# Kernel optimization log

Hardware: AMD Instinct MI355X
Metric: run time of the kernel (lower is better)

The kernel has to match this reference:

```python
import jax, jax.numpy as jnp
import numpy as np

N_NODES = 100000


def gcn_conv(x, src, dst, norm, W, b, n_nodes):
    # x: [N, Din]; src/dst: [E'] (with self-loops); norm: [E']
    h = x @ W  # [N, Dout] dense transform first (PyG GCNConv order)
    msgs = h[src] * norm[:, None]  # gather + degree scaling, [E', Dout]
    out = jax.ops.segment_sum(msgs, dst, num_segments=n_nodes)  # scatter-add
    return out + b


def setup_inputs() -> dict:
    key = jax.random.key(0)
    k_x, k_e, k_w1, k_w2 = jax.random.split(key, 4)
    input_dim, hidden_dim = 256, 128
    n_edges = 1600000
    x = jax.random.normal(k_x, (N_NODES, input_dim), dtype=jnp.float32)
    edge_index = jax.random.randint(k_e, (2, n_edges), 0, N_NODES, dtype=jnp.int64)
    # Glorot-style init for conv weights, zeros bias (PyG defaults)
    s1 = (6.0 / (input_dim + hidden_dim)) ** 0.5
    s2 = (6.0 / (hidden_dim + hidden_dim)) ** 0.5
    W1 = jax.random.uniform(k_w1, (input_dim, hidden_dim), jnp.float32, -s1, s1)
    W2 = jax.random.uniform(k_w2, (hidden_dim, hidden_dim), jnp.float32, -s2, s2)
    b1 = jnp.zeros((hidden_dim,), jnp.float32)
    b2 = jnp.zeros((hidden_dim,), jnp.float32)
    return {"x": x, "edge_index": edge_index, "W1": W1, "b1": b1, "W2": W2, "b2": b2}


def reference(x, edge_index, W1, b1, W2, b2):
    n = x.shape[0]
    loops = jnp.arange(n, dtype=edge_index.dtype)
    src = jnp.concatenate([edge_index[0], loops])  # add self-loops
    dst = jnp.concatenate([edge_index[1], loops])
    # symmetric normalization deg^-1/2 (in-degree including self-loops)
    deg = jax.ops.segment_sum(jnp.ones_like(dst, dtype=x.dtype), dst, num_segments=n)
    dinv = jax.lax.rsqrt(deg)
    norm = dinv[src] * dinv[dst]
    # layer 1: GCNConv -> ReLU (dropout is identity in eval mode)
    h = jax.nn.relu(gcn_conv(x, src, dst, norm, W1, b1, n))
    # layer 2
    h = jax.nn.relu(gcn_conv(h, src, dst, norm, W2, b2, n))
    return h
```

## Files before the change

kernel.cpp:

```cpp
#include <hip/hip_runtime.h>
#include <hip/hip_bf16.h>


#define DIN 256
#define DH 128
#define BKT_SHIFT 9
#define BKT_SZ 512
#define NBKT_MAX 256
#define CAP 10240

typedef __attribute__((ext_vector_type(8))) short short8;
typedef __attribute__((ext_vector_type(4))) float f32x4;
typedef __attribute__((ext_vector_type(2))) unsigned int uint2e;

__device__ __forceinline__ unsigned short f2bf(float f) {
    union { float f; unsigned int i; } c;
    c.f = f;
    unsigned int r = c.i + 0x7FFFu + ((c.i >> 16) & 1u);
    return (unsigned short)(r >> 16);
}
__device__ __forceinline__ float bf_lo(unsigned int u) {
    union { unsigned int i; float f; } c;
    c.i = u << 16;
    return c.f;
}
__device__ __forceinline__ float bf_hi(unsigned int u) {
    union { unsigned int i; float f; } c;
    c.i = u & 0xFFFF0000u;
    return c.f;
}

__global__ __launch_bounds__(256) void cvt_zero_k(const float* __restrict__ W1,
                                                  const float* __restrict__ W2,
                                                  unsigned short* __restrict__ Wt1,
                                                  unsigned short* __restrict__ Wt2,
                                                  int* __restrict__ bcnt, int WTB) {
    int bx = blockIdx.x;
    int t = threadIdx.x;
    if (bx >= WTB) {
        bcnt[t] = 0;
        return;
    }
    int i = bx * 256 + t;
    if (i < 256 * 128) {
        int k = i >> 7, nn = i & 127;
        Wt1[(size_t)nn * 256 + k] = f2bf(W1[i]);
    } else {
        int j = i - 256 * 128;
        int k = j >> 7, nn = j & 127;
        Wt2[(size_t)nn * 128 + k] = f2bf(W2[j]);
    }
}

template <bool A_BF16, bool SCALE>
__device__ __forceinline__ void gemm_body(unsigned short* Bt, int gb,
                                          const void* __restrict__ Av,
                                          const unsigned short* __restrict__ Wt,
                                          const float* __restrict__ dinv,
                                          unsigned short* __restrict__ Hb,
                                          int M, int K) {
    const int t = threadIdx.x;
    const int w = t >> 6;
    const int lane = t & 63;
    const int l15 = lane & 15;
    const int quad = lane >> 4;
    const int row0 = gb * 128 + w * 32;

    const float* Af = (const float*)Av;
    const unsigned short* Ab = (const unsigned short*)Av;

    f32x4 acc[2][8];
#pragma unroll
    for (int rt = 0; rt < 2; ++rt)
#pragma unroll
        for (int ct = 0; ct < 8; ++ct)
#pragma unroll
            for (int j = 0; j < 4; ++j) acc[rt][ct][j] = 0.0f;

    for (int kc = 0; kc < K; kc += 128) {
        if (kc) __syncthreads();
#pragma unroll
        for (int i = 0; i < 8; ++i) {
            int fg = w * 8 + i;
            int ks = fg >> 3, ct = fg & 7;
            int nn = ct * 16 + l15;
            int gk = ks * 32 + quad * 8;
            *(short8*)&Bt[fg * 512 + lane * 8] =
                *(const short8*)(Wt + (size_t)nn * K + kc + gk);
        }
        __syncthreads();
#pragma unroll
        for (int ks = 0; ks < 4; ++ks) {
            int kk = ks * 32 + quad * 8;
            short8 af[2];
#pragma unroll
            for (int rt = 0; rt < 2; ++rt) {
                int row = row0 + rt * 16 + l15;
                if (row < M) {
                    if (A_BF16) {
                        af[rt] = *(const short8*)(Ab + (size_t)row * K + kc + kk);
                    } else {
                        const float* p = Af + (size_t)row * K + kc + kk;
                        float4 x0 = *(const float4*)p;
                        float4 x1 = *(const float4*)(p + 4);
                        af[rt][0] = (short)f2bf(x0.x);
                        af[rt][1] = (short)f2bf(x0.y);
                        af[rt][2] = (short)f2bf(x0.z);
                        af[rt][3] = (short)f2bf(x0.w);
                        af[rt][4] = (short)f2bf(x1.x);
                        af[rt][5] = (short)f2bf(x1.y);
                        af[rt][6] = (short)f2bf(x1.z);
                        af[rt][7] = (short)f2bf(x1.w);
                    }
                } else {
#pragma unroll
                    for (int j = 0; j < 8; ++j) af[rt][j] = 0;
                }
            }
#pragma unroll
            for (int ct = 0; ct < 8; ++ct) {
                short8 bfr = *(const short8*)&Bt[(ks * 8 + ct) * 512 + lane * 8];
                acc[0][ct] = __builtin_amdgcn_mfma_f32_16x16x32_bf16(af[0], bfr, acc[0][ct], 0, 0, 0);
                acc[1][ct] = __builtin_amdgcn_mfma_f32_16x16x32_bf16(af[1], bfr, acc[1][ct], 0, 0, 0);
            }
        }
    }
#pragma unroll
    for (int rt = 0; rt < 2; ++rt)
#pragma unroll
        for (int r = 0; r < 4; ++r) {
            int row = row0 + rt * 16 + quad * 4 + r;
            if (row < M) {
                float dv = SCALE ? dinv[row] : 1.0f;
                unsigned short* o = Hb + (size_t)row * 128 + l15;
#pragma unroll
                for (int ct = 0; ct < 8; ++ct)
                    o[ct * 16] = f2bf(SCALE ? dv * acc[rt][ct][r] : acc[rt][ct][r]);
            }
        }
}

struct SmemFused {
    union {
        unsigned short Bt[16384];
        struct {
            int hist[NBKT_MAX];
            int rstart[NBKT_MAX];
        } bk;
    };
};

__global__ __launch_bounds__(256) void fused1_k(const int* __restrict__ src,
                                                const int* __restrict__ dst,
                                                int* __restrict__ bcnt,
                                                int* __restrict__ tmp, int e, int n,
                                                int NBB,
                                                const float* __restrict__ x,
                                                const unsigned short* __restrict__ Wt1,
                                                unsigned short* __restrict__ hb, int M) {
    __shared__ SmemFused sm;
    int bx = blockIdx.x;
    int t = threadIdx.x;
    if (bx < NBB) {
        int* hist = sm.bk.hist;
        int* rstart = sm.bk.rstart;
        int chunk = (e + NBB - 1) / NBB;
        int beg = bx * chunk, end = min(e, beg + chunk);

        hist[t] = 0;
        __syncthreads();
        for (int i = beg + t; i < end; i += 256) atomicAdd(&hist[dst[i] >> BKT_SHIFT], 1);
        __syncthreads();
        int nbkt = (n + BKT_SZ - 1) >> BKT_SHIFT;
        int h = hist[t];
        if (t < nbkt && h > 0) rstart[t] = atomicAdd(&bcnt[t], h);
        __syncthreads();
        hist[t] = 0;
        __syncthreads();
        for (int i = beg + t; i < end; i += 256) {
            int d = dst[i];
            int b = d >> BKT_SHIFT;
            int o = atomicAdd(&hist[b], 1);
            tmp[(size_t)b * CAP + rstart[b] + o] = src[i] | ((d & (BKT_SZ - 1)) << 20);
        }
        return;
    }
    gemm_body<false, false>(sm.Bt, bx - NBB, x, Wt1, nullptr, hb, M, DIN);
}

__global__ __launch_bounds__(1024) void scatter2_k(const int* __restrict__ tmp,
                                                   const int* __restrict__ bcnt,
                                                   float* __restrict__ dinv,
                                                   int* __restrict__ rowptr,
                                                   int* __restrict__ einfo, int n,
                                                   int nbkt) {
    __shared__ int hist[BKT_SZ];
    __shared__ int scn[BKT_SZ];
    __shared__ int cur[BKT_SZ];
    int b = blockIdx.x;
    int t = threadIdx.x;
    int lo = b << BKT_SHIFT;
    int nn = min(n - lo, BKT_SZ);
    int cnt = bcnt[b];
    const int* rec = tmp + (size_t)b * CAP;

    if (t < 256) scn[t] = (t < nbkt) ? bcnt[t] : 0;
    __syncthreads();
    for (int off = 1; off < 256; off <<= 1) {
        int v = 0;
        if (t < 256 && t >= off) v = scn[t - off];
        __syncthreads();
        if (t < 256) scn[t] += v;
        __syncthreads();
    }
    int bas = scn[b] - cnt;
    if (b == nbkt - 1 && t == 0) rowptr[n] = scn[nbkt - 1];
    __syncthreads();

    if (t < BKT_SZ) hist[t] = 0;
    __syncthreads();
    for (int i = t; i < cnt; i += 1024) atomicAdd(&hist[(rec[i] >> 20) & (BKT_SZ - 1)], 1);
    __syncthreads();
    if (t < BKT_SZ) scn[t] = hist[t];
    __syncthreads();
    for (int off = 1; off < BKT_SZ; off <<= 1) {
        int v = 0;
        if (t < BKT_SZ && t >= off) v = scn[t - off];
        __syncthreads();
        if (t < BKT_SZ) scn[t] += v;
        __syncthreads();
    }
    if (t < nn) {
        int excl = bas + scn[t] - hist[t];
        dinv[lo + t] = 1.0f / sqrtf((float)(hist[t] + 1));
        rowptr[lo + t] = excl;
        cur[t] = excl;
    }
    __syncthreads();
    for (int i = t; i < cnt; i += 1024) {
        int r = rec[i];
        int dlow = (r >> 20) & (BKT_SZ - 1);
        int pos = atomicAdd(&cur[dlow], 1);
        einfo[pos] = r & 0xFFFFF;
    }
}

template <bool SCALE_SRC, bool OUT_BF16>
__global__ __launch_bounds__(256, 8) void agg_k(const unsigned short* __restrict__ Hb,
                                                const int* __restrict__ rowptr,
                                                const int* __restrict__ einfo,
                                                const float* __restrict__ dinv,
                                                const float* __restrict__ bias,
                                                void* __restrict__ out, int n) {
    int v = blockIdx.x * 4 + (threadIdx.x >> 6);
    int lane = threadIdx.x & 63;
    if (v >= n) return;
    int l = lane & 31, half = lane >> 5;
    const uint2* __restrict__ H = (const uint2*)Hb;
    float dv = dinv[v];
    float a0 = 0.f, a1 = 0.f, a2 = 0.f, a3 = 0.f;
    if (half == 0) {
        uint2 hv = H[(size_t)v * 32 + l];
        if (SCALE_SRC) {
            a0 = dv * bf_lo(hv.x); a1 = dv * bf_hi(hv.x);
            a2 = dv * bf_lo(hv.y); a3 = dv * bf_hi(hv.y);
        } else {
            a0 = bf_lo(hv.x); a1 = bf_hi(hv.x);
            a2 = bf_lo(hv.y); a3 = bf_hi(hv.y);
        }
    }
    int end = rowptr[v + 1];
    int i = rowptr[v] + half;
    for (; i + 14 < end; i += 16) {
        int s0 = __builtin_nontemporal_load(&einfo[i]);
        int s1 = __builtin_nontemporal_load(&einfo[i + 2]);
        int s2 = __builtin_nontemporal_load(&einfo[i + 4]);
        int s3 = __builtin_nontemporal_load(&einfo[i + 6]);
        int s4 = __builtin_nontemporal_load(&einfo[i + 8]);
        int s5 = __builtin_nontemporal_load(&einfo[i + 10]);
        int s6 = __builtin_nontemporal_load(&einfo[i + 12]);
        int s7 = __builtin_nontemporal_load(&einfo[i + 14]);
        float d0 = 1.f, d1 = 1.f, d2 = 1.f, d3 = 1.f;
        float d4 = 1.f, d5 = 1.f, d6 = 1.f, d7 = 1.f;
        if (SCALE_SRC) {
            d0 = dinv[s0]; d1 = dinv[s1]; d2 = dinv[s2]; d3 = dinv[s3];
            d4 = dinv[s4]; d5 = dinv[s5]; d6 = dinv[s6]; d7 = dinv[s7];
        }
        uint2 v0 = H[(size_t)s0 * 32 + l];
        uint2 v1 = H[(size_t)s1 * 32 + l];
        uint2 v2 = H[(size_t)s2 * 32 + l];
        uint2 v3 = H[(size_t)s3 * 32 + l];
        uint2 v4 = H[(size_t)s4 * 32 + l];
        uint2 v5 = H[(size_t)s5 * 32 + l];
        uint2 v6 = H[(size_t)s6 * 32 + l];
        uint2 v7 = H[(size_t)s7 * 32 + l];
        if (SCALE_SRC) {
            a0 = fmaf(d0, bf_lo(v0.x), a0); a1 = fmaf(d0, bf_hi(v0.x), a1);
            a2 = fmaf(d0, bf_lo(v0.y), a2); a3 = fmaf(d0, bf_hi(v0.y), a3);
            a0 = fmaf(d1, bf_lo(v1.x), a0); a1 = fmaf(d1, bf_hi(v1.x), a1);
            a2 = fmaf(d1, bf_lo(v1.y), a2); a3 = fmaf(d1, bf_hi(v1.y), a3);
            a0 = fmaf(d2, bf_lo(v2.x), a0); a1 = fmaf(d2, bf_hi(v2.x), a1);
            a2 = fmaf(d2, bf_lo(v2.y), a2); a3 = fmaf(d2, bf_hi(v2.y), a3);
            a0 = fmaf(d3, bf_lo(v3.x), a0); a1 = fmaf(d3, bf_hi(v3.x), a1);
            a2 = fmaf(d3, bf_lo(v3.y), a2); a3 = fmaf(d3, bf_hi(v3.y), a3);
            a0 = fmaf(d4, bf_lo(v4.x), a0); a1 = fmaf(d4, bf_hi(v4.x), a1);
            a2 = fmaf(d4, bf_lo(v4.y), a2); a3 = fmaf(d4, bf_hi(v4.y), a3);
            a0 = fmaf(d5, bf_lo(v5.x), a0); a1 = fmaf(d5, bf_hi(v5.x), a1);
            a2 = fmaf(d5, bf_lo(v5.y), a2); a3 = fmaf(d5, bf_hi(v5.y), a3);
            a0 = fmaf(d6, bf_lo(v6.x), a0); a1 = fmaf(d6, bf_hi(v6.x), a1);
            a2 = fmaf(d6, bf_lo(v6.y), a2); a3 = fmaf(d6, bf_hi(v6.y), a3);
            a0 = fmaf(d7, bf_lo(v7.x), a0); a1 = fmaf(d7, bf_hi(v7.x), a1);
            a2 = fmaf(d7, bf_lo(v7.y), a2); a3 = fmaf(d7, bf_hi(v7.y), a3);
        } else {
            a0 += bf_lo(v0.x); a1 += bf_hi(v0.x); a2 += bf_lo(v0.y); a3 += bf_hi(v0.y);
            a0 += bf_lo(v1.x); a1 += bf_hi(v1.x); a2 += bf_lo(v1.y); a3 += bf_hi(v1.y);
            a0 += bf_lo(v2.x); a1 += bf_hi(v2.x); a2 += bf_lo(v2.y); a3 += bf_hi(v2.y);
            a0 += bf_lo(v3.x); a1 += bf_hi(v3.x); a2 += bf_lo(v3.y); a3 += bf_hi(v3.y);
            a0 += bf_lo(v4.x); a1 += bf_hi(v4.x); a2 += bf_lo(v4.y); a3 += bf_hi(v4.y);
            a0 += bf_lo(v5.x); a1 += bf_hi(v5.x); a2 += bf_lo(v5.y); a3 += bf_hi(v5.y);
            a0 += bf_lo(v6.x); a1 += bf_hi(v6.x); a2 += bf_lo(v6.y); a3 += bf_hi(v6.y);
            a0 += bf_lo(v7.x); a1 += bf_hi(v7.x); a2 += bf_lo(v7.y); a3 += bf_hi(v7.y);
        }
    }
    for (; i + 6 < end; i += 8) {
        int s0 = __builtin_nontemporal_load(&einfo[i]);
        int s1 = __builtin_nontemporal_load(&einfo[i + 2]);
        int s2 = __builtin_nontemporal_load(&einfo[i + 4]);
        int s3 = __builtin_nontemporal_load(&einfo[i + 6]);
        float d0 = 1.f, d1 = 1.f, d2 = 1.f, d3 = 1.f;
        if (SCALE_SRC) { d0 = dinv[s0]; d1 = dinv[s1]; d2 = dinv[s2]; d3 = dinv[s3]; }
        uint2 v0 = H[(size_t)s0 * 32 + l];
        uint2 v1 = H[(size_t)s1 * 32 + l];
        uint2 v2 = H[(size_t)s2 * 32 + l];
        uint2 v3 = H[(size_t)s3 * 32 + l];
        if (SCALE_SRC) {
            a0 = fmaf(d0, bf_lo(v0.x), a0); a1 = fmaf(d0, bf_hi(v0.x), a1);
            a2 = fmaf(d0, bf_lo(v0.y), a2); a3 = fmaf(d0, bf_hi(v0.y), a3);
            a0 = fmaf(d1, bf_lo(v1.x), a0); a1 = fmaf(d1, bf_hi(v1.x), a1);
            a2 = fmaf(d1, bf_lo(v1.y), a2); a3 = fmaf(d1, bf_hi(v1.y), a3);
            a0 = fmaf(d2, bf_lo(v2.x), a0); a1 = fmaf(d2, bf_hi(v2.x), a1);
            a2 = fmaf(d2, bf_lo(v2.y), a2); a3 = fmaf(d2, bf_hi(v2.y), a3);
            a0 = fmaf(d3, bf_lo(v3.x), a0); a1 = fmaf(d3, bf_hi(v3.x), a1);
            a2 = fmaf(d3, bf_lo(v3.y), a2); a3 = fmaf(d3, bf_hi(v3.y), a3);
        } else {
            a0 += bf_lo(v0.x); a1 += bf_hi(v0.x); a2 += bf_lo(v0.y); a3 += bf_hi(v0.y);
            a0 += bf_lo(v1.x); a1 += bf_hi(v1.x); a2 += bf_lo(v1.y); a3 += bf_hi(v1.y);
            a0 += bf_lo(v2.x); a1 += bf_hi(v2.x); a2 += bf_lo(v2.y); a3 += bf_hi(v2.y);
            a0 += bf_lo(v3.x); a1 += bf_hi(v3.x); a2 += bf_lo(v3.y); a3 += bf_hi(v3.y);
        }
    }
    for (; i < end; i += 2) {
        int s = __builtin_nontemporal_load(&einfo[i]);
        float ds = SCALE_SRC ? dinv[s] : 1.f;
        uint2 vv = H[(size_t)s * 32 + l];
        if (SCALE_SRC) {
            a0 = fmaf(ds, bf_lo(vv.x), a0); a1 = fmaf(ds, bf_hi(vv.x), a1);
            a2 = fmaf(ds, bf_lo(vv.y), a2); a3 = fmaf(ds, bf_hi(vv.y), a3);
        } else {
            a0 += bf_lo(vv.x); a1 += bf_hi(vv.x); a2 += bf_lo(vv.y); a3 += bf_hi(vv.y);
        }
    }
    a0 += __shfl_xor(a0, 32);
    a1 += __shfl_xor(a1, 32);
    a2 += __shfl_xor(a2, 32);
    a3 += __shfl_xor(a3, 32);
    if (half == 0) {
        float4 bb = ((const float4*)bias)[l];
        float o0 = fmaxf(fmaf(dv, a0, bb.x), 0.f);
        float o1 = fmaxf(fmaf(dv, a1, bb.y), 0.f);
        float o2 = fmaxf(fmaf(dv, a2, bb.z), 0.f);
        float o3 = fmaxf(fmaf(dv, a3, bb.w), 0.f);
        if (OUT_BF16) {
            uint2e p;
            p.x = (unsigned int)f2bf(o0) | ((unsigned int)f2bf(o1) << 16);
            p.y = (unsigned int)f2bf(o2) | ((unsigned int)f2bf(o3) << 16);
            __builtin_nontemporal_store(p, (uint2e*)out + (size_t)v * 32 + l);
        } else {
            f32x4 o = {o0, o1, o2, o3};
            __builtin_nontemporal_store(o, (f32x4*)out + (size_t)v * 32 + l);
        }
    }
}

__global__ __launch_bounds__(256) void gemm2_k(const unsigned short* __restrict__ A,
                                               const unsigned short* __restrict__ Wt,
                                               const float* __restrict__ dinv,
                                               unsigned short* __restrict__ Hb,
                                               int M, int K) {
    __shared__ unsigned short Bt[16384];
    gemm_body<true, true>(Bt, blockIdx.x, A, Wt, dinv, Hb, M, K);
}

static inline size_t align_up(size_t x, size_t a) { return (x + a - 1) & ~(a - 1); }

extern "C" void kernel_launch(void* const* d_in, const int* in_sizes, int n_in,
                              void* d_out, int out_size, void* d_ws, size_t ws_size,
                              hipStream_t stream) {
    const float* x  = (const float*)d_in[0];
    const int*   ei = (const int*)d_in[1];
    const float* W1 = (const float*)d_in[2];
    const float* b1 = (const float*)d_in[3];
    const float* W2 = (const float*)d_in[4];
    const float* b2 = (const float*)d_in[5];

    const int N = in_sizes[0] / DIN;
    const int E = in_sizes[1] / 2;
    const int* src = ei;
    const int* dst = ei + E;
    const int NBKT = (N + BKT_SZ - 1) >> BKT_SHIFT;

    char* base_p = (char*)d_ws;
    size_t off = 0;
    int* bcnt = (int*)(base_p + off);       off = align_up(off + 256 * 4, 256);
    int* rowptr = (int*)(base_p + off);     off = align_up(off + (size_t)(N + 1) * 4, 256);
    float* dinv = (float*)(base_p + off);   off = align_up(off + (size_t)N * 4, 256);
    int* tmp = (int*)(base_p + off);        off = align_up(off + (size_t)NBKT * CAP * 4, 256);
    int* einfo = (int*)(base_p + off);      off = align_up(off + (size_t)E * 4, 256);
    unsigned short* Wt1 = (unsigned short*)(base_p + off); off = align_up(off + (size_t)128 * 256 * 2, 256);
    unsigned short* Wt2 = (unsigned short*)(base_p + off); off = align_up(off + (size_t)128 * 128 * 2, 256);
    unsigned short* hb  = (unsigned short*)(base_p + off); off = align_up(off + (size_t)N * 128 * 2, 256);
    unsigned short* a1b = (unsigned short*)(base_p + off); off = align_up(off + (size_t)N * 128 * 2, 256);

    float* out = (float*)d_out;

    const int NBB = 512;
    const int WTB = (256 * 128 + 128 * 128 + 255) / 256;
    const int GB = (N + 127) / 128;

    cvt_zero_k<<<WTB + 1, 256, 0, stream>>>(W1, W2, Wt1, Wt2, bcnt, WTB);
    fused1_k<<<NBB + GB, 256, 0, stream>>>(src, dst, bcnt, tmp, E, N, NBB, x, Wt1, hb, N);
    scatter2_k<<<NBKT, 1024, 0, stream>>>(tmp, bcnt, dinv, rowptr, einfo, N, NBKT);
    agg_k<true, true><<<(N + 3) / 4, 256, 0, stream>>>(hb, rowptr, einfo, dinv, b1, a1b, N);
    gemm2_k<<<GB, 256, 0, stream>>>(a1b, Wt2, dinv, hb, N, DH);
    agg_k<false, false><<<(N + 3) / 4, 256, 0, stream>>>(hb, rowptr, einfo, dinv, b2, out, N);
}
```

Measured before the change: 408.8 us.

## Reorder layer 2 to aggregate first, then apply W2 inside aggregation kernel

Layer 2 now aggregates the layer-1 activations first and applies the W2 transform afterwards, using the associativity (A·H)·W = A·(H·W). The 128x128 matmul runs per node inside the aggregation kernel with fp32 FMAs and wave shuffles. This removes the separate gemm2 kernel, the bf16 round-trip of the intermediate H·W2, and the W2 conversion. The trade-off is a scalar-FMA matmul in each node's wave (128 shuffles and 128 W2 row reads per wave) instead of MFMA tensor ops.

```diff
diff --git a/kernel.cpp b/kernel.cpp
--- a/kernel.cpp
+++ b/kernel.cpp
@@ -11,6 +11,7 @@
 
 typedef __attribute__((ext_vector_type(8))) short short8;
 typedef __attribute__((ext_vector_type(4))) float f32x4;
+typedef __attribute__((ext_vector_type(2))) float f32x2;
 typedef __attribute__((ext_vector_type(2))) unsigned int uint2e;
 
 __device__ __forceinline__ unsigned short f2bf(float f) {
@@ -31,9 +32,7 @@
 }
 
 __global__ __launch_bounds__(256) void cvt_zero_k(const float* __restrict__ W1,
-                                                  const float* __restrict__ W2,
                                                   unsigned short* __restrict__ Wt1,
-                                                  unsigned short* __restrict__ Wt2,
                                                   int* __restrict__ bcnt, int WTB) {
     int bx = blockIdx.x;
     int t = threadIdx.x;
@@ -42,21 +41,13 @@
         return;
     }
     int i = bx * 256 + t;
-    if (i < 256 * 128) {
-        int k = i >> 7, nn = i & 127;
-        Wt1[(size_t)nn * 256 + k] = f2bf(W1[i]);
-    } else {
-        int j = i - 256 * 128;
-        int k = j >> 7, nn = j & 127;
-        Wt2[(size_t)nn * 128 + k] = f2bf(W2[j]);
-    }
-}
-
-template <bool A_BF16, bool SCALE>
+    int k = i >> 7, nn = i & 127;
+    Wt1[(size_t)nn * 256 + k] = f2bf(W1[i]);
+}
+
 __device__ __forceinline__ void gemm_body(unsigned short* Bt, int gb,
-                                          const void* __restrict__ Av,
+                                          const float* __restrict__ Af,
                                           const unsigned short* __restrict__ Wt,
-                                          const float* __restrict__ dinv,
                                           unsigned short* __restrict__ Hb,
                                           int M, int K) {
     const int t = threadIdx.x;
@@ -66,9 +57,6 @@
     const int quad = lane >> 4;
     const int row0 = gb * 128 + w * 32;
 
-    const float* Af = (const float*)Av;
-    const unsigned short* Ab = (const unsigned short*)Av;
-
     f32x4 acc[2][8];
 #pragma unroll
     for (int rt = 0; rt < 2; ++rt)
@@ -97,21 +85,17 @@
             for (int rt = 0; rt < 2; ++rt) {
                 int row = row0 + rt * 16 + l15;
                 if (row < M) {
-                    if (A_BF16) {
-                        af[rt] = *(const short8*)(Ab + (size_t)row * K + kc + kk);
-                    } else {
-                        const float* p = Af + (size_t)row * K + kc + kk;
-                        float4 x0 = *(const float4*)p;
-                        float4 x1 = *(const float4*)(p + 4);
-                        af[rt][0] = (short)f2bf(x0.x);
-                        af[rt][1] = (short)f2bf(x0.y);
-                        af[rt][2] = (short)f2bf(x0.z);
-                        af[rt][3] = (short)f2bf(x0.w);
-                        af[rt][4] = (short)f2bf(x1.x);
-                        af[rt][5] = (short)f2bf(x1.y);
-                        af[rt][6] = (short)f2bf(x1.z);
-                        af[rt][7] = (short)f2bf(x1.w);
-                    }
+                    const float* p = Af + (size_t)row * K + kc + kk;
+                    float4 x0 = *(const float4*)p;
+                    float4 x1 = *(const float4*)(p + 4);
+                    af[rt][0] = (short)f2bf(x0.x);
+                    af[rt][1] = (short)f2bf(x0.y);
+                    af[rt][2] = (short)f2bf(x0.z);
+                    af[rt][3] = (short)f2bf(x0.w);
+                    af[rt][4] = (short)f2bf(x1.x);
+                    af[rt][5] = (short)f2bf(x1.y);
+                    af[rt][6] = (short)f2bf(x1.z);
+                    af[rt][7] = (short)f2bf(x1.w);
                 } else {
 #pragma unroll
                     for (int j = 0; j < 8; ++j) af[rt][j] = 0;
@@ -131,11 +115,9 @@
         for (int r = 0; r < 4; ++r) {
             int row = row0 + rt * 16 + quad * 4 + r;
             if (row < M) {
-                float dv = SCALE ? dinv[row] : 1.0f;
                 unsigned short* o = Hb + (size_t)row * 128 + l15;
 #pragma unroll
-                for (int ct = 0; ct < 8; ++ct)
-                    o[ct * 16] = f2bf(SCALE ? dv * acc[rt][ct][r] : acc[rt][ct][r]);
+                for (int ct = 0; ct < 8; ++ct) o[ct * 16] = f2bf(acc[rt][ct][r]);
             }
         }
 }
@@ -185,7 +167,7 @@
         }
         return;
     }
-    gemm_body<false, false>(sm.Bt, bx - NBB, x, Wt1, nullptr, hb, M, DIN);
+    gemm_body(sm.Bt, bx - NBB, x, Wt1, hb, M, DIN);
 }
 
 __global__ __launch_bounds__(1024) void scatter2_k(const int* __restrict__ tmp,
@@ -245,29 +227,16 @@
     }
 }
 
-template <bool SCALE_SRC, bool OUT_BF16>
-__global__ __launch_bounds__(256, 8) void agg_k(const unsigned short* __restrict__ Hb,
-                                                const int* __restrict__ rowptr,
-                                                const int* __restrict__ einfo,
-                                                const float* __restrict__ dinv,
-                                                const float* __restrict__ bias,
-                                                void* __restrict__ out, int n) {
-    int v = blockIdx.x * 4 + (threadIdx.x >> 6);
-    int lane = threadIdx.x & 63;
-    if (v >= n) return;
-    int l = lane & 31, half = lane >> 5;
-    const uint2* __restrict__ H = (const uint2*)Hb;
-    float dv = dinv[v];
-    float a0 = 0.f, a1 = 0.f, a2 = 0.f, a3 = 0.f;
+__device__ __forceinline__ void gather_scaled(const uint2* __restrict__ H,
+                                              const int* __restrict__ rowptr,
+                                              const int* __restrict__ einfo,
+                                              const float* __restrict__ dinv,
+                                              int v, int l, int half, float dv,
+                                              float& a0, float& a1, float& a2, float& a3) {
     if (half == 0) {
         uint2 hv = H[(size_t)v * 32 + l];
-        if (SCALE_SRC) {
-            a0 = dv * bf_lo(hv.x); a1 = dv * bf_hi(hv.x);
-            a2 = dv * bf_lo(hv.y); a3 = dv * bf_hi(hv.y);
-        } else {
-            a0 = bf_lo(hv.x); a1 = bf_hi(hv.x);
-            a2 = bf_lo(hv.y); a3 = bf_hi(hv.y);
-        }
+        a0 = dv * bf_lo(hv.x); a1 = dv * bf_hi(hv.x);
+        a2 = dv * bf_lo(hv.y); a3 = dv * bf_hi(hv.y);
     }
     int end = rowptr[v + 1];
     int i = rowptr[v] + half;
@@ -280,12 +249,8 @@
         int s5 = __builtin_nontemporal_load(&einfo[i + 10]);
         int s6 = __builtin_nontemporal_load(&einfo[i + 12]);
         int s7 = __builtin_nontemporal_load(&einfo[i + 14]);
-        float d0 = 1.f, d1 = 1.f, d2 = 1.f, d3 = 1.f;
-        float d4 = 1.f, d5 = 1.f, d6 = 1.f, d7 = 1.f;
-        if (SCALE_SRC) {
-            d0 = dinv[s0]; d1 = dinv[s1]; d2 = dinv[s2]; d3 = dinv[s3];
-            d4 = dinv[s4]; d5 = dinv[s5]; d6 = dinv[s6]; d7 = dinv[s7];
-        }
+        float d0 = dinv[s0], d1 = dinv[s1], d2 = dinv[s2], d3 = dinv[s3];
+        float d4 = dinv[s4], d5 = dinv[s5], d6 = dinv[s6], d7 = dinv[s7];
         uint2 v0 = H[(size_t)s0 * 32 + l];
         uint2 v1 = H[(size_t)s1 * 32 + l];
         uint2 v2 = H[(size_t)s2 * 32 + l];
@@ -294,101 +259,118 @@
         uint2 v5 = H[(size_t)s5 * 32 + l];
         uint2 v6 = H[(size_t)s6 * 32 + l];
         uint2 v7 = H[(size_t)s7 * 32 + l];
-        if (SCALE_SRC) {
-            a0 = fmaf(d0, bf_lo(v0.x), a0); a1 = fmaf(d0, bf_hi(v0.x), a1);
-            a2 = fmaf(d0, bf_lo(v0.y), a2); a3 = fmaf(d0, bf_hi(v0.y), a3);
-            a0 = fmaf(d1, bf_lo(v1.x), a0); a1 = fmaf(d1, bf_hi(v1.x), a1);
-            a2 = fmaf(d1, bf_lo(v1.y), a2); a3 = fmaf(d1, bf_hi(v1.y), a3);
-            a0 = fmaf(d2, bf_lo(v2.x), a0); a1 = fmaf(d2, bf_hi(v2.x), a1);
-            a2 = fmaf(d2, bf_lo(v2.y), a2); a3 = fmaf(d2, bf_hi(v2.y), a3);
-            a0 = fmaf(d3, bf_lo(v3.x), a0); a1 = fmaf(d3, bf_hi(v3.x), a1);
-            a2 = fmaf(d3, bf_lo(v3.y), a2); a3 = fmaf(d3, bf_hi(v3.y), a3);
-            a0 = fmaf(d4, bf_lo(v4.x), a0); a1 = fmaf(d4, bf_hi(v4.x), a1);
-            a2 = fmaf(d4, bf_lo(v4.y), a2); a3 = fmaf(d4, bf_hi(v4.y), a3);
-            a0 = fmaf(d5, bf_lo(v5.x), a0); a1 = fmaf(d5, bf_hi(v5.x), a1);
-            a2 = fmaf(d5, bf_lo(v5.y), a2); a3 = fmaf(d5, bf_hi(v5.y), a3);
-            a0 = fmaf(d6, bf_lo(v6.x), a0); a1 = fmaf(d6, bf_hi(v6.x), a1);
-            a2 = fmaf(d6, bf_lo(v6.y), a2); a3 = fmaf(d6, bf_hi(v6.y), a3);
-            a0 = fmaf(d7, bf_lo(v7.x), a0); a1 = fmaf(d7, bf_hi(v7.x), a1);
-            a2 = fmaf(d7, bf_lo(v7.y), a2); a3 = fmaf(d7, bf_hi(v7.y), a3);
-        } else {
-            a0 += bf_lo(v0.x); a1 += bf_hi(v0.x); a2 += bf_lo(v0.y); a3 += bf_hi(v0.y);
-            a0 += bf_lo(v1.x); a1 += bf_hi(v1.x); a2 += bf_lo(v1.y); a3 += bf_hi(v1.y);
-            a0 += bf_lo(v2.x); a1 += bf_hi(v2.x); a2 += bf_lo(v2.y); a3 += bf_hi(v2.y);
-            a0 += bf_lo(v3.x); a1 += bf_hi(v3.x); a2 += bf_lo(v3.y); a3 += bf_hi(v3.y);
-            a0 += bf_lo(v4.x); a1 += bf_hi(v4.x); a2 += bf_lo(v4.y); a3 += bf_hi(v4.y);
-            a0 += bf_lo(v5.x); a1 += bf_hi(v5.x); a2 += bf_lo(v5.y); a3 += bf_hi(v5.y);
-            a0 += bf_lo(v6.x); a1 += bf_hi(v6.x); a2 += bf_lo(v6.y); a3 += bf_hi(v6.y);
-            a0 += bf_lo(v7.x); a1 += bf_hi(v7.x); a2 += bf_lo(v7.y); a3 += bf_hi(v7.y);
-        }
+        a0 = fmaf(d0, bf_lo(v0.x), a0); a1 = fmaf(d0, bf_hi(v0.x), a1);
+        a2 = fmaf(d0, bf_lo(v0.y), a2); a3 = fmaf(d0, bf_hi(v0.y), a3);
+        a0 = fmaf(d1, bf_lo(v1.x), a0); a1 = fmaf(d1, bf_hi(v1.x), a1);
+        a2 = fmaf(d1, bf_lo(v1.y), a2); a3 = fmaf(d1, bf_hi(v1.y), a3);
+        a0 = fmaf(d2, bf_lo(v2.x), a0); a1 = fmaf(d2, bf_hi(v2.x), a1);
+        a2 = fmaf(d2, bf_lo(v2.y), a2); a3 = fmaf(d2, bf_hi(v2.y), a3);
+        a0 = fmaf(d3, bf_lo(v3.x), a0); a1 = fmaf(d3, bf_hi(v3.x), a1);
+        a2 = fmaf(d3, bf_lo(v3.y), a2); a3 = fmaf(d3, bf_hi(v3.y), a3);
+        a0 = fmaf(d4, bf_lo(v4.x), a0); a1 = fmaf(d4, bf_hi(v4.x), a1);
+        a2 = fmaf(d4, bf_lo(v4.y), a2); a3 = fmaf(d4, bf_hi(v4.y), a3);
+        a0 = fmaf(d5, bf_lo(v5.x), a0); a1 = fmaf(d5, bf_hi(v5.x), a1);
+        a2 = fmaf(d5, bf_lo(v5.y), a2); a3 = fmaf(d5, bf_hi(v5.y), a3);
+        a0 = fmaf(d6, bf_lo(v6.x), a0); a1 = fmaf(d6, bf_hi(v6.x), a1);
+        a2 = fmaf(d6, bf_lo(v6.y), a2); a3 = fmaf(d6, bf_hi(v6.y), a3);
+        a0 = fmaf(d7, bf_lo(v7.x), a0); a1 = fmaf(d7, bf_hi(v7.x), a1);
+        a2 = fmaf(d7, bf_lo(v7.y), a2); a3 = fmaf(d7, bf_hi(v7.y), a3);
     }
     for (; i + 6 < end; i += 8) {
         int s0 = __builtin_nontemporal_load(&einfo[i]);
         int s1 = __builtin_nontemporal_load(&einfo[i + 2]);
         int s2 = __builtin_nontemporal_load(&einfo[i + 4]);
         int s3 = __builtin_nontemporal_load(&einfo[i + 6]);
-        float d0 = 1.f, d1 = 1.f, d2 = 1.f, d3 = 1.f;
-        if (SCALE_SRC) { d0 = dinv[s0]; d1 = dinv[s1]; d2 = dinv[s2]; d3 = dinv[s3]; }
+        float d0 = dinv[s0], d1 = dinv[s1], d2 = dinv[s2], d3 = dinv[s3];
         uint2 v0 = H[(size_t)s0 * 32 + l];
         uint2 v1 = H[(size_t)s1 * 32 + l];
         uint2 v2 = H[(size_t)s2 * 32 + l];
         uint2 v3 = H[(size_t)s3 * 32 + l];
-        if (SCALE_SRC) {
-            a0 = fmaf(d0, bf_lo(v0.x), a0); a1 = fmaf(d0, bf_hi(v0.x), a1);
-            a2 = fmaf(d0, bf_lo(v0.y), a2); a3 = fmaf(d0, bf_hi(v0.y), a3);
-            a0 = fmaf(d1, bf_lo(v1.x), a0); a1 = fmaf(d1, bf_hi(v1.x), a1);
-            a2 = fmaf(d1, bf_lo(v1.y), a2); a3 = fmaf(d1, bf_hi(v1.y), a3);
-            a0 = fmaf(d2, bf_lo(v2.x), a0); a1 = fmaf(d2, bf_hi(v2.x), a1);
-            a2 = fmaf(d2, bf_lo(v2.y), a2); a3 = fmaf(d2, bf_hi(v2.y), a3);
-            a0 = fmaf(d3, bf_lo(v3.x), a0); a1 = fmaf(d3, bf_hi(v3.x), a1);
-            a2 = fmaf(d3, bf_lo(v3.y), a2); a3 = fmaf(d3, bf_hi(v3.y), a3);
-        } else {
-            a0 += bf_lo(v0.x); a1 += bf_hi(v0.x); a2 += bf_lo(v0.y); a3 += bf_hi(v0.y);
-            a0 += bf_lo(v1.x); a1 += bf_hi(v1.x); a2 += bf_lo(v1.y); a3 += bf_hi(v1.y);
-            a0 += bf_lo(v2.x); a1 += bf_hi(v2.x); a2 += bf_lo(v2.y); a3 += bf_hi(v2.y);
-            a0 += bf_lo(v3.x); a1 += bf_hi(v3.x); a2 += bf_lo(v3.y); a3 += bf_hi(v3.y);
-        }
+        a0 = fmaf(d0, bf_lo(v0.x), a0); a1 = fmaf(d0, bf_hi(v0.x), a1);
+        a2 = fmaf(d0, bf_lo(v0.y), a2); a3 = fmaf(d0, bf_hi(v0.y), a3);
+        a0 = fmaf(d1, bf_lo(v1.x), a0); a1 = fmaf(d1, bf_hi(v1.x), a1);
+        a2 = fmaf(d1, bf_lo(v1.y), a2); a3 = fmaf(d1, bf_hi(v1.y), a3);
+        a0 = fmaf(d2, bf_lo(v2.x), a0); a1 = fmaf(d2, bf_hi(v2.x), a1);
+        a2 = fmaf(d2, bf_lo(v2.y), a2); a3 = fmaf(d2, bf_hi(v2.y), a3);
+        a0 = fmaf(d3, bf_lo(v3.x), a0); a1 = fmaf(d3, bf_hi(v3.x), a1);
+        a2 = fmaf(d3, bf_lo(v3.y), a2); a3 = fmaf(d3, bf_hi(v3.y), a3);
     }
     for (; i < end; i += 2) {
         int s = __builtin_nontemporal_load(&einfo[i]);
-        float ds = SCALE_SRC ? dinv[s] : 1.f;
+        float ds = dinv[s];
         uint2 vv = H[(size_t)s * 32 + l];
-        if (SCALE_SRC) {
-            a0 = fmaf(ds, bf_lo(vv.x), a0); a1 = fmaf(ds, bf_hi(vv.x), a1);
-            a2 = fmaf(ds, bf_lo(vv.y), a2); a3 = fmaf(ds, bf_hi(vv.y), a3);
-        } else {
-            a0 += bf_lo(vv.x); a1 += bf_hi(vv.x); a2 += bf_lo(vv.y); a3 += bf_hi(vv.y);
-        }
+        a0 = fmaf(ds, bf_lo(vv.x), a0); a1 = fmaf(ds, bf_hi(vv.x), a1);
+        a2 = fmaf(ds, bf_lo(vv.y), a2); a3 = fmaf(ds, bf_hi(vv.y), a3);
     }
     a0 += __shfl_xor(a0, 32);
     a1 += __shfl_xor(a1, 32);
     a2 += __shfl_xor(a2, 32);
     a3 += __shfl_xor(a3, 32);
+}
+
+__global__ __launch_bounds__(256, 8) void agg1_k(const unsigned short* __restrict__ Hb,
+                                                 const int* __restrict__ rowptr,
+                                                 const int* __restrict__ einfo,
+                                                 const float* __restrict__ dinv,
+                                                 const float* __restrict__ bias,
+                                                 unsigned short* __restrict__ out, int n) {
+    int v = blockIdx.x * 4 + (threadIdx.x >> 6);
+    int lane = threadIdx.x & 63;
+    if (v >= n) return;
+    int l = lane & 31, half = lane >> 5;
+    float dv = dinv[v];
+    float a0 = 0.f, a1 = 0.f, a2 = 0.f, a3 = 0.f;
+    gather_scaled((const uint2*)Hb, rowptr, einfo, dinv, v, l, half, dv, a0, a1, a2, a3);
     if (half == 0) {
         float4 bb = ((const float4*)bias)[l];
         float o0 = fmaxf(fmaf(dv, a0, bb.x), 0.f);
         float o1 = fmaxf(fmaf(dv, a1, bb.y), 0.f);
         float o2 = fmaxf(fmaf(dv, a2, bb.z), 0.f);
         float o3 = fmaxf(fmaf(dv, a3, bb.w), 0.f);
-        if (OUT_BF16) {
-            uint2e p;
-            p.x = (unsigned int)f2bf(o0) | ((unsigned int)f2bf(o1) << 16);
-            p.y = (unsigned int)f2bf(o2) | ((unsigned int)f2bf(o3) << 16);
-            __builtin_nontemporal_store(p, (uint2e*)out + (size_t)v * 32 + l);
-        } else {
-            f32x4 o = {o0, o1, o2, o3};
-            __builtin_nontemporal_store(o, (f32x4*)out + (size_t)v * 32 + l);
-        }
-    }
-}
-
-__global__ __launch_bounds__(256) void gemm2_k(const unsigned short* __restrict__ A,
-                                               const unsigned short* __restrict__ Wt,
-                                               const float* __restrict__ dinv,
-                                               unsigned short* __restrict__ Hb,
-                                               int M, int K) {
-    __shared__ unsigned short Bt[16384];
-    gemm_body<true, true>(Bt, blockIdx.x, A, Wt, dinv, Hb, M, K);
+        uint2e p;
+        p.x = (unsigned int)f2bf(o0) | ((unsigned int)f2bf(o1) << 16);
+        p.y = (unsigned int)f2bf(o2) | ((unsigned int)f2bf(o3) << 16);
+        __builtin_nontemporal_store(p, (uint2e*)out + (size_t)v * 32 + l);
+    }
+}
+
+__global__ __launch_bounds__(256, 8) void agg2_w2_k(const unsigned short* __restrict__ A,
+                                                    const int* __restrict__ rowptr,
+                                                    const int* __restrict__ einfo,
+                                                    const float* __restrict__ dinv,
+                                                    const float* __restrict__ W2,
+                                                    const float* __restrict__ b2,
+                                                    float* __restrict__ out, int n) {
+    int v = blockIdx.x * 4 + (threadIdx.x >> 6);
+    int lane = threadIdx.x & 63;
+    if (v >= n) return;
+    int l = lane & 31, half = lane >> 5;
+    float dv = dinv[v];
+    float a0 = 0.f, a1 = 0.f, a2 = 0.f, a3 = 0.f;
+    gather_scaled((const uint2*)A, rowptr, einfo, dinv, v, l, half, dv, a0, a1, a2, a3);
+    a0 *= dv; a1 *= dv; a2 *= dv; a3 *= dv;
+    float o0 = b2[2 * lane];
+    float o1 = b2[2 * lane + 1];
+#pragma unroll 4
+    for (int kq = 0; kq < 32; ++kq) {
+        float y0 = __shfl(a0, kq);
+        float y1 = __shfl(a1, kq);
+        float y2 = __shfl(a2, kq);
+        float y3 = __shfl(a3, kq);
+        const float* wr = W2 + (size_t)(4 * kq) * 128 + 2 * lane;
+        f32x2 w0 = *(const f32x2*)(wr);
+        f32x2 w1 = *(const f32x2*)(wr + 128);
+        f32x2 w2 = *(const f32x2*)(wr + 256);
+        f32x2 w3 = *(const f32x2*)(wr + 384);
+        o0 = fmaf(y0, w0.x, o0); o1 = fmaf(y0, w0.y, o1);
+        o0 = fmaf(y1, w1.x, o0); o1 = fmaf(y1, w1.y, o1);
+        o0 = fmaf(y2, w2.x, o0); o1 = fmaf(y2, w2.y, o1);
+        o0 = fmaf(y3, w3.x, o0); o1 = fmaf(y3, w3.y, o1);
+    }
+    o0 = fmaxf(o0, 0.f);
+    o1 = fmaxf(o1, 0.f);
+    f32x2 ov = {o0, o1};
+    __builtin_nontemporal_store(ov, (f32x2*)(out + (size_t)v * 128) + lane);
 }
 
 static inline size_t align_up(size_t x, size_t a) { return (x + a - 1) & ~(a - 1); }
@@ -417,20 +399,18 @@
     int* tmp = (int*)(base_p + off);        off = align_up(off + (size_t)NBKT * CAP * 4, 256);
     int* einfo = (int*)(base_p + off);      off = align_up(off + (size_t)E * 4, 256);
     unsigned short* Wt1 = (unsigned short*)(base_p + off); off = align_up(off + (size_t)128 * 256 * 2, 256);
-    unsigned short* Wt2 = (unsigned short*)(base_p + off); off = align_up(off + (size_t)128 * 128 * 2, 256);
     unsigned short* hb  = (unsigned short*)(base_p + off); off = align_up(off + (size_t)N * 128 * 2, 256);
     unsigned short* a1b = (unsigned short*)(base_p + off); off = align_up(off + (size_t)N * 128 * 2, 256);
 
     float* out = (float*)d_out;
 
     const int NBB = 512;
-    const int WTB = (256 * 128 + 128 * 128 + 255) / 256;
+    const int WTB = (256 * 128) / 256;
     const int GB = (N + 127) / 128;
 
-    cvt_zero_k<<<WTB + 1, 256, 0, stream>>>(W1, W2, Wt1, Wt2, bcnt, WTB);
+    cvt_zero_k<<<WTB + 1, 256, 0, stream>>>(W1, Wt1, bcnt, WTB);
     fused1_k<<<NBB + GB, 256, 0, stream>>>(src, dst, bcnt, tmp, E, N, NBB, x, Wt1, hb, N);
     scatter2_k<<<NBKT, 1024, 0, stream>>>(tmp, bcnt, dinv, rowptr, einfo, N, NBKT);
-    agg_k<true, true><<<(N + 3) / 4, 256, 0, stream>>>(hb, rowptr, einfo, dinv, b1, a1b, N);
-    gemm2_k<<<GB, 256, 0, stream>>>(a1b, Wt2, dinv, hb, N, DH);
-    agg_k<false, false><<<(N + 3) / 4, 256, 0, stream>>>(hb, rowptr, einfo, dinv, b2, out, N);
-}
+    agg1_k<<<(N + 3) / 4, 256, 0, stream>>>(hb, rowptr, einfo, dinv, b1, a1b, N);
+    agg2_w2_k<<<(N + 3) / 4, 256, 0, stream>>>(a1b, rowptr, einfo, dinv, W2, b2, out, N);
+}
```

Result: slower. 724.8 us (+77.3%).
